# Performance work log

Hardware: AMD Instinct MI355X
Metric: run time of the kernel (lower is better)

The kernel has to match this reference:

```python
import jax, jax.numpy as jnp
import numpy as np

B, Q, K, H, DQ, DK, DV = 16, 128, 512, 128, 128, 128, 128
MASK_VALUE = -1000000.0  # matches d2l.sequence_mask fill value


def setup_inputs() -> dict:
    key = jax.random.key(0)
    ks = jax.random.split(key, 7)
    queries = jax.random.normal(ks[0], (B, Q, DQ), dtype=jnp.float32)
    keys = jax.random.normal(ks[1], (B, K, DK), dtype=jnp.float32)
    values = jax.random.normal(ks[2], (B, K, DV), dtype=jnp.float32)
    valid_lens = jax.random.randint(ks[3], (B,), 1, K + 1, dtype=jnp.int32)
    # Linear params (no bias), scaled like torch default init ~ 1/sqrt(fan_in)
    W_q = jax.random.normal(ks[4], (DQ, H), dtype=jnp.float32) / np.sqrt(DQ)
    W_k = jax.random.normal(ks[5], (DK, H), dtype=jnp.float32) / np.sqrt(DK)
    w_v = jax.random.normal(ks[6], (H,), dtype=jnp.float32) / np.sqrt(H)
    return {"queries": queries, "keys": keys, "values": values,
            "valid_lens": valid_lens, "W_q": W_q, "W_k": W_k, "w_v": w_v}


def reference(queries, keys, values, valid_lens, W_q, W_k, w_v):
    # Project queries and keys: (B,Q,H), (B,K,H)
    q = jnp.einsum("bqd,dh->bqh", queries, W_q)
    k = jnp.einsum("bkd,dh->bkh", keys, W_k)
    # Broadcast add -> tanh -> linear-to-1 score: (B,Q,K)
    features = jnp.tanh(q[:, :, None, :] + k[:, None, :, :])  # (B,Q,K,H)
    scores = jnp.einsum("bqkh,h->bqk", features, w_v)
    # masked softmax over last axis; valid_lens is (B,), broadcast over Q
    mask = jnp.arange(K)[None, None, :] < valid_lens[:, None, None]  # (B,1,K)
    scores = jnp.where(mask, scores, MASK_VALUE)
    attn = jax.nn.softmax(scores, axis=-1)
    # weighted sum over keys: (B,Q,DV)
    return jnp.einsum("bqk,bkv->bqv", attn, values)
```

## Files before the change

### kernel.cpp

```cpp
#include <hip/hip_runtime.h>

#define NB 16
#define NQ 128
#define NK 512
#define NH 128
#define NDV 128

#define KPAD 132

typedef __attribute__((ext_vector_type(8))) short short8;
typedef __attribute__((ext_vector_type(4))) float f32x4;
typedef __attribute__((ext_vector_type(2))) float f32x2;

#define C2LOG2E 2.8853900817779268f
#define LOG2E   1.4426950408889634f

__device__ __forceinline__ short f2bf(float x) {
    unsigned u = __float_as_uint(x);
    unsigned r = (u + 0x7fffu + ((u >> 16) & 1u)) >> 16;
    return (short)r;
}
__device__ __forceinline__ float bf2f(short s) {
    return __uint_as_float(((unsigned)(unsigned short)s) << 16);
}

__global__ __launch_bounds__(256) void wsplit_kernel(
    const float* __restrict__ Wq, const float* __restrict__ Wk,
    const float* __restrict__ wv,
    short* __restrict__ pqh, short* __restrict__ pql,
    short* __restrict__ pkh, short* __restrict__ pkl,
    float* __restrict__ w2)
{
    int blk = blockIdx.x;
    int t   = threadIdx.x;
    if (blk == 0 && t < NH) w2[t] = 2.0f * wv[t];
    int w = blk >> 3, ht = blk & 7;
    int ks = t >> 6, lane = t & 63;
    int m = lane & 15, quad = lane >> 4;
    const float* W = w ? Wk : Wq;
    short* ph = w ? pkh : pqh;
    short* pl = w ? pkl : pql;
    short8 hi, lo;
#pragma unroll
    for (int j = 0; j < 8; ++j) {
        float x = W[(size_t)(ks * 32 + quad * 8 + j) * NH + ht * 16 + m];
        short h = f2bf(x);
        hi[j] = h;
        lo[j] = f2bf(x - bf2f(h));
    }
    size_t o = (size_t)((ht * 4 + ks) * 64 + lane) * 8;
    *(short8*)(ph + o) = hi;
    *(short8*)(pl + o) = lo;
}

__global__ __launch_bounds__(256) void proj_kernel(
    const float* __restrict__ Xq, const float* __restrict__ Xk,
    const short* __restrict__ pqh, const short* __restrict__ pql,
    const short* __restrict__ pkh, const short* __restrict__ pkl,
    float* __restrict__ Eq, float* __restrict__ Ek)
{
    int blk = blockIdx.x;
    const float* X; const short* ph; const short* pl; float* Y; int row0;
    if (blk < 128) { X = Xq; ph = pqh; pl = pql; Y = Eq; row0 = blk * 16; }
    else           { X = Xk; ph = pkh; pl = pkl; Y = Ek; row0 = (blk - 128) * 16; }
    int t = threadIdx.x;
    int wave = t >> 6, lane = t & 63;
    int m = lane & 15, quad = lane >> 4;

    short8 AH[4], AL[4];
    const float* xr = X + (size_t)(row0 + m) * NH + quad * 8;
#pragma unroll
    for (int ks = 0; ks < 4; ++ks) {
#pragma unroll
        for (int j = 0; j < 8; ++j) {
            float x = xr[ks * 32 + j];
            short h = f2bf(x);
            AH[ks][j] = h;
            AL[ks][j] = f2bf(x - bf2f(h));
        }
    }
#pragma unroll
    for (int hi = 0; hi < 2; ++hi) {
        int ht = wave * 2 + hi;
        f32x4 acc = {0.f, 0.f, 0.f, 0.f};
#pragma unroll
        for (int ks = 0; ks < 4; ++ks) {
            size_t o = (size_t)((ht * 4 + ks) * 64 + lane) * 8;
            short8 bh = *(const short8*)(ph + o);
            short8 bl = *(const short8*)(pl + o);
            acc = __builtin_amdgcn_mfma_f32_16x16x32_bf16(AH[ks], bl, acc, 0, 0, 0);
            acc = __builtin_amdgcn_mfma_f32_16x16x32_bf16(AL[ks], bh, acc, 0, 0, 0);
            acc = __builtin_amdgcn_mfma_f32_16x16x32_bf16(AH[ks], bh, acc, 0, 0, 0);
        }
#pragma unroll
        for (int r = 0; r < 4; ++r)
            Y[(size_t)(row0 + quad * 4 + r) * NH + ht * 16 + m] =
                __builtin_amdgcn_exp2f(acc[r] * C2LOG2E);
    }
}

__global__ __launch_bounds__(512) void score_kernel(
    const float* __restrict__ Eqp, const float* __restrict__ Ekp,
    const int* __restrict__ vlen, const float* __restrict__ w2,
    float* __restrict__ P)
{
    __shared__ float s_ek[128 * KPAD];
    __shared__ float s_qw[8 * NH * 2];

    int blk = blockIdx.x;
    int b    = blk & 15;
    int rest = blk >> 4;
    int qt = rest & 15, kc = rest >> 4;
    int q0 = qt * 8, k0 = kc * 128;
    int t  = threadIdx.x;

    int nv = vlen[b];
    nv = max(1, min(NK, nv));
    float* Pb = P + ((size_t)b * NQ + q0) * NK;

    if (k0 >= nv) {
        int q = t >> 6, kk = (t & 63) * 2;
        f32x2 z = {0.f, 0.f};
        *(f32x2*)&Pb[(size_t)q * NK + k0 + kk] = z;
        return;
    }

    for (int i = t; i < 128 * 32; i += 512) {
        int row = i >> 5, c4 = i & 31;
        *(f32x4*)&s_ek[row * KPAD + c4 * 4] =
            *(const f32x4*)&Ekp[((size_t)b * NK + k0 + row) * NH + c4 * 4];
    }
    for (int i = t; i < 8 * NH; i += 512) {
        int q = i >> 7, h = i & 127;
        s_qw[i * 2]     = Eqp[((size_t)b * NQ + q0 + q) * NH + h];
        s_qw[i * 2 + 1] = w2[h];
    }
    __syncthreads();

    int lane = t & 63, wave = t >> 6;

    float s2 = w2[lane] + w2[lane + 64];
#pragma unroll
    for (int off = 32; off; off >>= 1) s2 += __shfl_xor(s2, off);
    float wsum = 0.5f * s2;

    const float* e1 = &s_ek[lane * KPAD];
    const float* e2 = &s_ek[(lane + 64) * KPAD];
    const float* qw = &s_qw[wave * NH * 2];

    float c0 = 0.f, c1 = 0.f, c2 = 0.f, c3 = 0.f;
    float c4 = 0.f, c5 = 0.f, c6 = 0.f, c7 = 0.f;
#pragma unroll
    for (int hh = 0; hh < NH; hh += 8) {
        f32x4 p0 = *(const f32x4*)(qw + hh * 2);
        f32x4 p1 = *(const f32x4*)(qw + hh * 2 + 4);
        f32x4 p2 = *(const f32x4*)(qw + hh * 2 + 8);
        f32x4 p3 = *(const f32x4*)(qw + hh * 2 + 12);
        f32x4 kA = *(const f32x4*)(e1 + hh);
        f32x4 kB = *(const f32x4*)(e1 + hh + 4);
        f32x4 kC = *(const f32x4*)(e2 + hh);
        f32x4 kD = *(const f32x4*)(e2 + hh + 4);
        c0 = fmaf(p0[1], __builtin_amdgcn_rcpf(fmaf(p0[0], kA[0], 1.0f)), c0);
        c1 = fmaf(p0[3], __builtin_amdgcn_rcpf(fmaf(p0[2], kA[1], 1.0f)), c1);
        c2 = fmaf(p1[1], __builtin_amdgcn_rcpf(fmaf(p1[0], kA[2], 1.0f)), c2);
        c3 = fmaf(p1[3], __builtin_amdgcn_rcpf(fmaf(p1[2], kA[3], 1.0f)), c3);
        c4 = fmaf(p0[1], __builtin_amdgcn_rcpf(fmaf(p0[0], kC[0], 1.0f)), c4);
        c5 = fmaf(p0[3], __builtin_amdgcn_rcpf(fmaf(p0[2], kC[1], 1.0f)), c5);
        c6 = fmaf(p1[1], __builtin_amdgcn_rcpf(fmaf(p1[0], kC[2], 1.0f)), c6);
        c7 = fmaf(p1[3], __builtin_amdgcn_rcpf(fmaf(p1[2], kC[3], 1.0f)), c7);
        c0 = fmaf(p2[1], __builtin_amdgcn_rcpf(fmaf(p2[0], kB[0], 1.0f)), c0);
        c1 = fmaf(p2[3], __builtin_amdgcn_rcpf(fmaf(p2[2], kB[1], 1.0f)), c1);
        c2 = fmaf(p3[1], __builtin_amdgcn_rcpf(fmaf(p3[0], kB[2], 1.0f)), c2);
        c3 = fmaf(p3[3], __builtin_amdgcn_rcpf(fmaf(p3[2], kB[3], 1.0f)), c3);
        c4 = fmaf(p2[1], __builtin_amdgcn_rcpf(fmaf(p2[0], kD[0], 1.0f)), c4);
        c5 = fmaf(p2[3], __builtin_amdgcn_rcpf(fmaf(p2[2], kD[1], 1.0f)), c5);
        c6 = fmaf(p3[1], __builtin_amdgcn_rcpf(fmaf(p3[0], kD[2], 1.0f)), c6);
        c7 = fmaf(p3[3], __builtin_amdgcn_rcpf(fmaf(p3[2], kD[3], 1.0f)), c7);
    }
    float sc1 = wsum - ((c0 + c1) + (c2 + c3));
    float sc2 = wsum - ((c4 + c5) + (c6 + c7));
    int k1 = k0 + lane, k2 = k0 + 64 + lane;
    float pp1 = (k1 < nv) ? __builtin_amdgcn_exp2f(sc1 * LOG2E) : 0.f;
    float pp2 = (k2 < nv) ? __builtin_amdgcn_exp2f(sc2 * LOG2E) : 0.f;
    float* Pr = Pb + (size_t)wave * NK;
    Pr[k1] = pp1;
    Pr[k2] = pp2;
}

__global__ __launch_bounds__(512) void av_kernel(
    const float* __restrict__ P, const float* __restrict__ V,
    const int* __restrict__ vlen, float* __restrict__ out)
{
    __shared__ float s_p[4 * NK];
    __shared__ float s_red[8 * 64 * 2];
    __shared__ float s_sum[8];

    int blk = blockIdx.x;
    int b = blk & 15, qt = blk >> 4;
    int q0 = qt * 4;
    int t = threadIdx.x;

    int nv = vlen[b];
    nv = max(1, min(NK, nv));

    const f32x4* Pv = (const f32x4*)(P + ((size_t)b * NQ + q0) * NK);
    ((f32x4*)s_p)[t] = Pv[t];
    __syncthreads();

    int lane = t & 63, w = t >> 6;
    int q = w & 3, half = w >> 2;
    int kbeg = half * 256, kend = min(nv, kbeg + 256);
    const float* pr = &s_p[q * NK];

    f32x4 u = *(const f32x4*)(pr + kbeg + lane * 4);
    float sm = (u[0] + u[1]) + (u[2] + u[3]);
#pragma unroll
    for (int off = 32; off; off >>= 1) sm += __shfl_xor(sm, off);
    if (lane == 0) s_sum[w] = sm;

    int dv0 = lane * 2;
    const float* Vb = V + (size_t)b * NK * NDV + dv0;
    float o0 = 0.f, o1 = 0.f;
    int k = kbeg;
    for (; k + 8 <= kend; k += 8) {
        f32x4 pA = *(const f32x4*)(pr + k);
        f32x4 pB = *(const f32x4*)(pr + k + 4);
        f32x2 v0 = *(const f32x2*)(Vb + (size_t)(k + 0) * NDV);
        f32x2 v1 = *(const f32x2*)(Vb + (size_t)(k + 1) * NDV);
        f32x2 v2 = *(const f32x2*)(Vb + (size_t)(k + 2) * NDV);
        f32x2 v3 = *(const f32x2*)(Vb + (size_t)(k + 3) * NDV);
        f32x2 v4 = *(const f32x2*)(Vb + (size_t)(k + 4) * NDV);
        f32x2 v5 = *(const f32x2*)(Vb + (size_t)(k + 5) * NDV);
        f32x2 v6 = *(const f32x2*)(Vb + (size_t)(k + 6) * NDV);
        f32x2 v7 = *(const f32x2*)(Vb + (size_t)(k + 7) * NDV);
        o0 = fmaf(pA[0], v0[0], o0); o1 = fmaf(pA[0], v0[1], o1);
        o0 = fmaf(pA[1], v1[0], o0); o1 = fmaf(pA[1], v1[1], o1);
        o0 = fmaf(pA[2], v2[0], o0); o1 = fmaf(pA[2], v2[1], o1);
        o0 = fmaf(pA[3], v3[0], o0); o1 = fmaf(pA[3], v3[1], o1);
        o0 = fmaf(pB[0], v4[0], o0); o1 = fmaf(pB[0], v4[1], o1);
        o0 = fmaf(pB[1], v5[0], o0); o1 = fmaf(pB[1], v5[1], o1);
        o0 = fmaf(pB[2], v6[0], o0); o1 = fmaf(pB[2], v6[1], o1);
        o0 = fmaf(pB[3], v7[0], o0); o1 = fmaf(pB[3], v7[1], o1);
    }
    for (; k < kend; ++k) {
        float p = pr[k];
        f32x2 v = *(const f32x2*)(Vb + (size_t)k * NDV);
        o0 = fmaf(p, v[0], o0);
        o1 = fmaf(p, v[1], o1);
    }
    f32x2 po = {o0, o1};
    *(f32x2*)&s_red[(w * 64 + lane) * 2] = po;
    __syncthreads();

    if (w < 4) {
        f32x2 x0 = *(const f32x2*)&s_red[(w * 64 + lane) * 2];
        f32x2 x1 = *(const f32x2*)&s_red[((w + 4) * 64 + lane) * 2];
        float rinv = 1.0f / (s_sum[w] + s_sum[w + 4]);
        size_t ob = ((size_t)b * NQ + q0 + w) * NDV + dv0;
        f32x2 o = {(x0[0] + x1[0]) * rinv, (x0[1] + x1[1]) * rinv};
        *(f32x2*)&out[ob] = o;
    }
}

extern "C" void kernel_launch(void* const* d_in, const int* in_sizes, int n_in,
                              void* d_out, int out_size, void* d_ws, size_t ws_size,
                              hipStream_t stream) {
    const float* q  = (const float*)d_in[0];
    const float* ks = (const float*)d_in[1];
    const float* vs = (const float*)d_in[2];
    const int*   vl = (const int*)d_in[3];
    const float* wq = (const float*)d_in[4];
    const float* wk = (const float*)d_in[5];
    const float* wv = (const float*)d_in[6];

    float* Eq = (float*)d_ws;
    float* Ek = Eq + 2048 * 128;
    float* P  = Ek + (size_t)8192 * 128;
    float* w2 = P + (size_t)NB * NQ * NK;
    short* pqh = (short*)(w2 + 128);
    short* pql = pqh + 16384;
    short* pkh = pql + 16384;
    short* pkl = pkh + 16384;

    wsplit_kernel<<<16, 256, 0, stream>>>(wq, wk, wv, pqh, pql, pkh, pkl, w2);
    proj_kernel<<<640, 256, 0, stream>>>(q, ks, pqh, pql, pkh, pkl, Eq, Ek);
    score_kernel<<<1024, 512, 0, stream>>>(Eq, Ek, vl, w2, P);
    av_kernel<<<512, 512, 0, stream>>>(P, vs, vl, (float*)d_out);
}
```

Baseline: 118.9 us.

## Retile score and AV kernels for register reuse; stage projection inputs in LDS

The score kernel now handles 16 queries per block, and each thread computes 4 queries against one key. Each loaded key vector is reused across several queries, and w2 is read from its own shared array instead of being interleaved. The AV kernel now handles 8 queries per block, with each wave doing two queries over the full key range, which removes the cross-wave reduction and its barrier. Each loaded V value is reused for two queries. The projection kernel stages its X tile through LDS with coalesced vector loads. In exchange there are fewer blocks, which lowers parallelism, and the AV loop is now sequential over the whole key range per wave.

```diff
diff --git a/kernel.cpp b/kernel.cpp
--- a/kernel.cpp
+++ b/kernel.cpp
@@ -59,6 +59,8 @@
     const short* __restrict__ pkh, const short* __restrict__ pkl,
     float* __restrict__ Eq, float* __restrict__ Ek)
 {
+    __shared__ float s_x[16 * KPAD];
+
     int blk = blockIdx.x;
     const float* X; const short* ph; const short* pl; float* Y; int row0;
     if (blk < 128) { X = Xq; ph = pqh; pl = pql; Y = Eq; row0 = blk * 16; }
@@ -67,16 +69,27 @@
     int wave = t >> 6, lane = t & 63;
     int m = lane & 15, quad = lane >> 4;
 
+#pragma unroll
+    for (int r = 0; r < 2; ++r) {
+        int i = (t + r * 256) * 4;
+        int row = i >> 7, col = i & 127;
+        *(f32x4*)&s_x[row * KPAD + col] =
+            *(const f32x4*)&X[(size_t)(row0 + row) * NH + col];
+    }
+    __syncthreads();
+
     short8 AH[4], AL[4];
-    const float* xr = X + (size_t)(row0 + m) * NH + quad * 8;
 #pragma unroll
     for (int ks = 0; ks < 4; ++ks) {
-#pragma unroll
-        for (int j = 0; j < 8; ++j) {
-            float x = xr[ks * 32 + j];
-            short h = f2bf(x);
-            AH[ks][j] = h;
-            AL[ks][j] = f2bf(x - bf2f(h));
+        int base = m * KPAD + ks * 32 + quad * 8;
+        f32x4 x0 = *(const f32x4*)&s_x[base];
+        f32x4 x1 = *(const f32x4*)&s_x[base + 4];
+#pragma unroll
+        for (int j = 0; j < 4; ++j) {
+            short h0 = f2bf(x0[j]);
+            AH[ks][j] = h0; AL[ks][j] = f2bf(x0[j] - bf2f(h0));
+            short h1 = f2bf(x1[j]);
+            AH[ks][j + 4] = h1; AL[ks][j + 4] = f2bf(x1[j] - bf2f(h1));
         }
     }
 #pragma unroll
@@ -105,13 +118,14 @@
     float* __restrict__ P)
 {
     __shared__ float s_ek[128 * KPAD];
-    __shared__ float s_qw[8 * NH * 2];
+    __shared__ float s_eq[16 * NH];
+    __shared__ float s_w2[NH];
 
     int blk = blockIdx.x;
     int b    = blk & 15;
     int rest = blk >> 4;
-    int qt = rest & 15, kc = rest >> 4;
-    int q0 = qt * 8, k0 = kc * 128;
+    int qt = rest & 7, kc = rest >> 3;
+    int q0 = qt * 16, k0 = kc * 128;
     int t  = threadIdx.x;
 
     int nv = vlen[b];
@@ -119,9 +133,9 @@
     float* Pb = P + ((size_t)b * NQ + q0) * NK;
 
     if (k0 >= nv) {
-        int q = t >> 6, kk = (t & 63) * 2;
-        f32x2 z = {0.f, 0.f};
-        *(f32x2*)&Pb[(size_t)q * NK + k0 + kk] = z;
+        int q = t >> 5, kk = (t & 31) * 4;
+        f32x4 z = {0.f, 0.f, 0.f, 0.f};
+        *(f32x4*)&Pb[(size_t)q * NK + k0 + kk] = z;
         return;
     }
 
@@ -130,101 +144,111 @@
         *(f32x4*)&s_ek[row * KPAD + c4 * 4] =
             *(const f32x4*)&Ekp[((size_t)b * NK + k0 + row) * NH + c4 * 4];
     }
-    for (int i = t; i < 8 * NH; i += 512) {
-        int q = i >> 7, h = i & 127;
-        s_qw[i * 2]     = Eqp[((size_t)b * NQ + q0 + q) * NH + h];
-        s_qw[i * 2 + 1] = w2[h];
-    }
+    *(f32x4*)&s_eq[t * 4] =
+        *(const f32x4*)&Eqp[((size_t)b * NQ + q0) * NH + t * 4];
+    if (t < 32) *(f32x4*)&s_w2[t * 4] = *(const f32x4*)&w2[t * 4];
     __syncthreads();
 
-    int lane = t & 63, wave = t >> 6;
-
-    float s2 = w2[lane] + w2[lane + 64];
+    int lane = t & 63, w = t >> 6;
+    int g = w & 3, hf = w >> 2;
+
+    float s2 = s_w2[lane] + s_w2[lane + 64];
 #pragma unroll
     for (int off = 32; off; off >>= 1) s2 += __shfl_xor(s2, off);
     float wsum = 0.5f * s2;
 
-    const float* e1 = &s_ek[lane * KPAD];
-    const float* e2 = &s_ek[(lane + 64) * KPAD];
-    const float* qw = &s_qw[wave * NH * 2];
-
-    float c0 = 0.f, c1 = 0.f, c2 = 0.f, c3 = 0.f;
-    float c4 = 0.f, c5 = 0.f, c6 = 0.f, c7 = 0.f;
+    const float* ek = &s_ek[(hf * 64 + lane) * KPAD];
+    const float* e0 = &s_eq[(g * 4 + 0) * NH];
+    const float* e1 = &s_eq[(g * 4 + 1) * NH];
+    const float* e2 = &s_eq[(g * 4 + 2) * NH];
+    const float* e3 = &s_eq[(g * 4 + 3) * NH];
+
+    float c00 = 0.f, c01 = 0.f, c10 = 0.f, c11 = 0.f;
+    float c20 = 0.f, c21 = 0.f, c30 = 0.f, c31 = 0.f;
 #pragma unroll
     for (int hh = 0; hh < NH; hh += 8) {
-        f32x4 p0 = *(const f32x4*)(qw + hh * 2);
-        f32x4 p1 = *(const f32x4*)(qw + hh * 2 + 4);
-        f32x4 p2 = *(const f32x4*)(qw + hh * 2 + 8);
-        f32x4 p3 = *(const f32x4*)(qw + hh * 2 + 12);
-        f32x4 kA = *(const f32x4*)(e1 + hh);
-        f32x4 kB = *(const f32x4*)(e1 + hh + 4);
-        f32x4 kC = *(const f32x4*)(e2 + hh);
-        f32x4 kD = *(const f32x4*)(e2 + hh + 4);
-        c0 = fmaf(p0[1], __builtin_amdgcn_rcpf(fmaf(p0[0], kA[0], 1.0f)), c0);
-        c1 = fmaf(p0[3], __builtin_amdgcn_rcpf(fmaf(p0[2], kA[1], 1.0f)), c1);
-        c2 = fmaf(p1[1], __builtin_amdgcn_rcpf(fmaf(p1[0], kA[2], 1.0f)), c2);
-        c3 = fmaf(p1[3], __builtin_amdgcn_rcpf(fmaf(p1[2], kA[3], 1.0f)), c3);
-        c4 = fmaf(p0[1], __builtin_amdgcn_rcpf(fmaf(p0[0], kC[0], 1.0f)), c4);
-        c5 = fmaf(p0[3], __builtin_amdgcn_rcpf(fmaf(p0[2], kC[1], 1.0f)), c5);
-        c6 = fmaf(p1[1], __builtin_amdgcn_rcpf(fmaf(p1[0], kC[2], 1.0f)), c6);
-        c7 = fmaf(p1[3], __builtin_amdgcn_rcpf(fmaf(p1[2], kC[3], 1.0f)), c7);
-        c0 = fmaf(p2[1], __builtin_amdgcn_rcpf(fmaf(p2[0], kB[0], 1.0f)), c0);
-        c1 = fmaf(p2[3], __builtin_amdgcn_rcpf(fmaf(p2[2], kB[1], 1.0f)), c1);
-        c2 = fmaf(p3[1], __builtin_amdgcn_rcpf(fmaf(p3[0], kB[2], 1.0f)), c2);
-        c3 = fmaf(p3[3], __builtin_amdgcn_rcpf(fmaf(p3[2], kB[3], 1.0f)), c3);
-        c4 = fmaf(p2[1], __builtin_amdgcn_rcpf(fmaf(p2[0], kD[0], 1.0f)), c4);
-        c5 = fmaf(p2[3], __builtin_amdgcn_rcpf(fmaf(p2[2], kD[1], 1.0f)), c5);
-        c6 = fmaf(p3[1], __builtin_amdgcn_rcpf(fmaf(p3[0], kD[2], 1.0f)), c6);
-        c7 = fmaf(p3[3], __builtin_amdgcn_rcpf(fmaf(p3[2], kD[3], 1.0f)), c7);
-    }
-    float sc1 = wsum - ((c0 + c1) + (c2 + c3));
-    float sc2 = wsum - ((c4 + c5) + (c6 + c7));
-    int k1 = k0 + lane, k2 = k0 + 64 + lane;
-    float pp1 = (k1 < nv) ? __builtin_amdgcn_exp2f(sc1 * LOG2E) : 0.f;
-    float pp2 = (k2 < nv) ? __builtin_amdgcn_exp2f(sc2 * LOG2E) : 0.f;
-    float* Pr = Pb + (size_t)wave * NK;
-    Pr[k1] = pp1;
-    Pr[k2] = pp2;
-}
-
-__global__ __launch_bounds__(512) void av_kernel(
+        f32x4 kA = *(const f32x4*)(ek + hh);
+        f32x4 kB = *(const f32x4*)(ek + hh + 4);
+        f32x4 wA = *(const f32x4*)(s_w2 + hh);
+        f32x4 wB = *(const f32x4*)(s_w2 + hh + 4);
+        f32x4 qA0 = *(const f32x4*)(e0 + hh), qB0 = *(const f32x4*)(e0 + hh + 4);
+        f32x4 qA1 = *(const f32x4*)(e1 + hh), qB1 = *(const f32x4*)(e1 + hh + 4);
+        f32x4 qA2 = *(const f32x4*)(e2 + hh), qB2 = *(const f32x4*)(e2 + hh + 4);
+        f32x4 qA3 = *(const f32x4*)(e3 + hh), qB3 = *(const f32x4*)(e3 + hh + 4);
+#pragma unroll
+        for (int i = 0; i < 4; ++i) {
+            c00 = fmaf(wA[i], __builtin_amdgcn_rcpf(fmaf(qA0[i], kA[i], 1.0f)), c00);
+            c10 = fmaf(wA[i], __builtin_amdgcn_rcpf(fmaf(qA1[i], kA[i], 1.0f)), c10);
+            c20 = fmaf(wA[i], __builtin_amdgcn_rcpf(fmaf(qA2[i], kA[i], 1.0f)), c20);
+            c30 = fmaf(wA[i], __builtin_amdgcn_rcpf(fmaf(qA3[i], kA[i], 1.0f)), c30);
+            c01 = fmaf(wB[i], __builtin_amdgcn_rcpf(fmaf(qB0[i], kB[i], 1.0f)), c01);
+            c11 = fmaf(wB[i], __builtin_amdgcn_rcpf(fmaf(qB1[i], kB[i], 1.0f)), c11);
+            c21 = fmaf(wB[i], __builtin_amdgcn_rcpf(fmaf(qB2[i], kB[i], 1.0f)), c21);
+            c31 = fmaf(wB[i], __builtin_amdgcn_rcpf(fmaf(qB3[i], kB[i], 1.0f)), c31);
+        }
+    }
+    int kg = k0 + hf * 64 + lane;
+    bool valid = kg < nv;
+    float p0 = valid ? __builtin_amdgcn_exp2f((wsum - (c00 + c01)) * LOG2E) : 0.f;
+    float p1 = valid ? __builtin_amdgcn_exp2f((wsum - (c10 + c11)) * LOG2E) : 0.f;
+    float p2 = valid ? __builtin_amdgcn_exp2f((wsum - (c20 + c21)) * LOG2E) : 0.f;
+    float p3 = valid ? __builtin_amdgcn_exp2f((wsum - (c30 + c31)) * LOG2E) : 0.f;
+    float* Pr = Pb + (size_t)(g * 4) * NK + kg;
+    Pr[0 * NK] = p0;
+    Pr[1 * NK] = p1;
+    Pr[2 * NK] = p2;
+    Pr[3 * NK] = p3;
+}
+
+__global__ __launch_bounds__(256) void av_kernel(
     const float* __restrict__ P, const float* __restrict__ V,
     const int* __restrict__ vlen, float* __restrict__ out)
 {
-    __shared__ float s_p[4 * NK];
-    __shared__ float s_red[8 * 64 * 2];
-    __shared__ float s_sum[8];
+    __shared__ float s_p[8 * NK];
 
     int blk = blockIdx.x;
     int b = blk & 15, qt = blk >> 4;
-    int q0 = qt * 4;
+    int q0 = qt * 8;
     int t = threadIdx.x;
 
     int nv = vlen[b];
     nv = max(1, min(NK, nv));
+    int nv8 = (nv + 7) & ~7;
 
     const f32x4* Pv = (const f32x4*)(P + ((size_t)b * NQ + q0) * NK);
-    ((f32x4*)s_p)[t] = Pv[t];
+#pragma unroll
+    for (int r = 0; r < 4; ++r)
+        ((f32x4*)s_p)[t + r * 256] = Pv[t + r * 256];
     __syncthreads();
 
     int lane = t & 63, w = t >> 6;
-    int q = w & 3, half = w >> 2;
-    int kbeg = half * 256, kend = min(nv, kbeg + 256);
-    const float* pr = &s_p[q * NK];
-
-    f32x4 u = *(const f32x4*)(pr + kbeg + lane * 4);
-    float sm = (u[0] + u[1]) + (u[2] + u[3]);
-#pragma unroll
-    for (int off = 32; off; off >>= 1) sm += __shfl_xor(sm, off);
-    if (lane == 0) s_sum[w] = sm;
+    int qa = w * 2, qb = qa + 1;
+    const float* pa = &s_p[qa * NK];
+    const float* pb = &s_p[qb * NK];
+
+    f32x4 sa0 = *(const f32x4*)(pa + lane * 8);
+    f32x4 sa1 = *(const f32x4*)(pa + lane * 8 + 4);
+    f32x4 sb0 = *(const f32x4*)(pb + lane * 8);
+    f32x4 sb1 = *(const f32x4*)(pb + lane * 8 + 4);
+    float sa = ((sa0[0] + sa0[1]) + (sa0[2] + sa0[3])) +
+               ((sa1[0] + sa1[1]) + (sa1[2] + sa1[3]));
+    float sb = ((sb0[0] + sb0[1]) + (sb0[2] + sb0[3])) +
+               ((sb1[0] + sb1[1]) + (sb1[2] + sb1[3]));
+#pragma unroll
+    for (int off = 32; off; off >>= 1) {
+        sa += __shfl_xor(sa, off);
+        sb += __shfl_xor(sb, off);
+    }
+    float ra = 1.0f / sa, rb = 1.0f / sb;
 
     int dv0 = lane * 2;
     const float* Vb = V + (size_t)b * NK * NDV + dv0;
-    float o0 = 0.f, o1 = 0.f;
-    int k = kbeg;
-    for (; k + 8 <= kend; k += 8) {
-        f32x4 pA = *(const f32x4*)(pr + k);
-        f32x4 pB = *(const f32x4*)(pr + k + 4);
+    float a0 = 0.f, a1 = 0.f, b0 = 0.f, b1 = 0.f;
+    for (int k = 0; k < nv8; k += 8) {
+        f32x4 PA0 = *(const f32x4*)(pa + k);
+        f32x4 PA1 = *(const f32x4*)(pa + k + 4);
+        f32x4 PB0 = *(const f32x4*)(pb + k);
+        f32x4 PB1 = *(const f32x4*)(pb + k + 4);
         f32x2 v0 = *(const f32x2*)(Vb + (size_t)(k + 0) * NDV);
         f32x2 v1 = *(const f32x2*)(Vb + (size_t)(k + 1) * NDV);
         f32x2 v2 = *(const f32x2*)(Vb + (size_t)(k + 2) * NDV);
@@ -233,33 +257,29 @@
         f32x2 v5 = *(const f32x2*)(Vb + (size_t)(k + 5) * NDV);
         f32x2 v6 = *(const f32x2*)(Vb + (size_t)(k + 6) * NDV);
         f32x2 v7 = *(const f32x2*)(Vb + (size_t)(k + 7) * NDV);
-        o0 = fmaf(pA[0], v0[0], o0); o1 = fmaf(pA[0], v0[1], o1);
-        o0 = fmaf(pA[1], v1[0], o0); o1 = fmaf(pA[1], v1[1], o1);
-        o0 = fmaf(pA[2], v2[0], o0); o1 = fmaf(pA[2], v2[1], o1);
-        o0 = fmaf(pA[3], v3[0], o0); o1 = fmaf(pA[3], v3[1], o1);
-        o0 = fmaf(pB[0], v4[0], o0); o1 = fmaf(pB[0], v4[1], o1);
-        o0 = fmaf(pB[1], v5[0], o0); o1 = fmaf(pB[1], v5[1], o1);
-        o0 = fmaf(pB[2], v6[0], o0); o1 = fmaf(pB[2], v6[1], o1);
-        o0 = fmaf(pB[3], v7[0], o0); o1 = fmaf(pB[3], v7[1], o1);
-    }
-    for (; k < kend; ++k) {
-        float p = pr[k];
-        f32x2 v = *(const f32x2*)(Vb + (size_t)k * NDV);
-        o0 = fmaf(p, v[0], o0);
-        o1 = fmaf(p, v[1], o1);
-    }
-    f32x2 po = {o0, o1};
-    *(f32x2*)&s_red[(w * 64 + lane) * 2] = po;
-    __syncthreads();
-
-    if (w < 4) {
-        f32x2 x0 = *(const f32x2*)&s_red[(w * 64 + lane) * 2];
-        f32x2 x1 = *(const f32x2*)&s_red[((w + 4) * 64 + lane) * 2];
-        float rinv = 1.0f / (s_sum[w] + s_sum[w + 4]);
-        size_t ob = ((size_t)b * NQ + q0 + w) * NDV + dv0;
-        f32x2 o = {(x0[0] + x1[0]) * rinv, (x0[1] + x1[1]) * rinv};
-        *(f32x2*)&out[ob] = o;
-    }
+        a0 = fmaf(PA0[0], v0[0], a0); a1 = fmaf(PA0[0], v0[1], a1);
+        b0 = fmaf(PB0[0], v0[0], b0); b1 = fmaf(PB0[0], v0[1], b1);
+        a0 = fmaf(PA0[1], v1[0], a0); a1 = fmaf(PA0[1], v1[1], a1);
+        b0 = fmaf(PB0[1], v1[0], b0); b1 = fmaf(PB0[1], v1[1], b1);
+        a0 = fmaf(PA0[2], v2[0], a0); a1 = fmaf(PA0[2], v2[1], a1);
+        b0 = fmaf(PB0[2], v2[0], b0); b1 = fmaf(PB0[2], v2[1], b1);
+        a0 = fmaf(PA0[3], v3[0], a0); a1 = fmaf(PA0[3], v3[1], a1);
+        b0 = fmaf(PB0[3], v3[0], b0); b1 = fmaf(PB0[3], v3[1], b1);
+        a0 = fmaf(PA1[0], v4[0], a0); a1 = fmaf(PA1[0], v4[1], a1);
+        b0 = fmaf(PB1[0], v4[0], b0); b1 = fmaf(PB1[0], v4[1], b1);
+        a0 = fmaf(PA1[1], v5[0], a0); a1 = fmaf(PA1[1], v5[1], a1);
+        b0 = fmaf(PB1[1], v5[0], b0); b1 = fmaf(PB1[1], v5[1], b1);
+        a0 = fmaf(PA1[2], v6[0], a0); a1 = fmaf(PA1[2], v6[1], a1);
+        b0 = fmaf(PB1[2], v6[0], b0); b1 = fmaf(PB1[2], v6[1], b1);
+        a0 = fmaf(PA1[3], v7[0], a0); a1 = fmaf(PA1[3], v7[1], a1);
+        b0 = fmaf(PB1[3], v7[0], b0); b1 = fmaf(PB1[3], v7[1], b1);
+    }
+    size_t oa = ((size_t)b * NQ + q0 + qa) * NDV + dv0;
+    size_t ob = ((size_t)b * NQ + q0 + qb) * NDV + dv0;
+    f32x2 Oa = {a0 * ra, a1 * ra};
+    f32x2 Ob = {b0 * rb, b1 * rb};
+    *(f32x2*)&out[oa] = Oa;
+    *(f32x2*)&out[ob] = Ob;
 }
 
 extern "C" void kernel_launch(void* const* d_in, const int* in_sizes, int n_in,
@@ -284,6 +304,6 @@
 
     wsplit_kernel<<<16, 256, 0, stream>>>(wq, wk, wv, pqh, pql, pkh, pkl, w2);
     proj_kernel<<<640, 256, 0, stream>>>(q, ks, pqh, pql, pkh, pkl, Eq, Ek);
-    score_kernel<<<1024, 512, 0, stream>>>(Eq, Ek, vl, w2, P);
-    av_kernel<<<512, 512, 0, stream>>>(P, vs, vl, (float*)d_out);
-}
+    score_kernel<<<512, 512, 0, stream>>>(Eq, Ek, vl, w2, P);
+    av_kernel<<<256, 256, 0, stream>>>(P, vs, vl, (float*)d_out);
+}
```

New measurement: 107.9 us. 1.1x faster.
